# Kernel tuning notes

Hardware: AMD Instinct MI355X
Metric: run time of the kernel (lower is better)

## Reference

```python
import jax, jax.numpy as jnp
import numpy as np

S = 128          # shared sequence length of v/q/a/k
D = 512          # model dim
H = 8            # n_heads
W = D // H       # head width (becomes the v/q/a einsum axes)
NUM = S // 8     # num_v = num_q = num_a = num_k
SCALE = float(np.sqrt(H))  # source divides by sqrt(a.size(-1)) == sqrt(n_heads)


def _heads(x):
    # split_last(x,(H,-1)).transpose(1,2) on a 2D (S,D) tensor -> (S, W, H)
    return x.reshape(S, H, W).transpose(0, 2, 1)


def setup_inputs() -> dict:
    key = jax.random.key(0)
    ks = jax.random.split(key, 24)
    d = {}
    for i, n in enumerate(['v', 'q', 'a', 'k']):
        d[n] = jax.random.normal(ks[i], (S, D), jnp.float32)
    for n in ['v_mask', 'q_mask', 'a_mask', 'k_mask']:
        d[n] = jnp.ones((S,), jnp.bool_)
    wnames = ['Wv', 'Wq', 'Wa', 'Wk', 'Wvo', 'Wqo', 'Wao', 'Wko']
    bnames = ['bv', 'bq', 'ba', 'bk', 'bvo', 'bqo', 'bao', 'bko']
    for i, (wn, bn) in enumerate(zip(wnames, bnames)):
        d[wn] = jax.random.normal(ks[4 + 2 * i], (D, D), jnp.float32) / np.sqrt(D)
        d[bn] = jax.random.normal(ks[5 + 2 * i], (D,), jnp.float32) * 0.01
    return d


def reference(v, q, a, k, v_mask, q_mask, a_mask, k_mask,
              Wv, bv, Wq, bq, Wa, ba, Wk, bk,
              Wvo, bvo, Wqo, bqo, Wao, bao, Wko, bko):
    # input projections (torch Linear: x @ W.T + b)
    vp = v @ Wv.T + bv
    qp = q @ Wq.T + bq
    ap = a @ Wa.T + ba
    kp = k @ Wk.T + bk
    # output projections are applied to the already-projected tensors
    vo = vp @ Wvo.T + bvo
    qo = qp @ Wqo.T + bqo
    ao = ap @ Wao.T + bao
    ko = kp @ Wko.T + bko
    tv, tq, ta, tk = map(_heads, (vp, qp, ap, kp))      # (S, W, H)
    tvo, tqo, tao, tko = map(_heads, (vo, qo, ao, ko))  # (S, W, H)
    # trilinear scores: in source labels b=1, h=S, v/q/a in W, w=H
    att = jnp.einsum('sic,sjc,slc->sijl', tv, tq, ta) / SCALE   # (S, W, W, W)
    att1 = jnp.einsum('sic,sjc,slc->sijl', tv, tq, tk) / SCALE  # (S, W, W, W)
    # joint softmax over the flat num_v*num_q*num_a axis (flat memory reshape,
    # exactly like torch .view); dropout p=0.0 -> identity
    scores = jax.nn.softmax(att.reshape(-1, H, NUM * NUM * NUM), axis=-1)
    scores = scores.reshape(-1, H, NUM, NUM, NUM)  # stored as self.scores in torch
    # output contractions use the UNNORMALIZED att1 (as in the source)
    v_res = jnp.einsum('sijl,sic->isc', att1, tvo).reshape(1, W, S * H)
    q_res = jnp.einsum('sijl,sjc->jsc', att1, tqo).reshape(1, W, S * H)
    a_res = jnp.einsum('sijl,slc->lsc', att1, tao).reshape(1, W, S * H)
    k_res = tko[None].reshape(1, S, W * H)
    return (v_res, q_res, a_res, k_res, scores)
```

## Files before the change

kernel.cpp:

```cpp
#include <hip/hip_runtime.h>
#include <hip/hip_bf16.h>

#define INV_SCALE 0.35355339059327373f

struct Proj4Args {
  const float* x[4];
  const float* w[4];
  const float* b[4];
  float* y[4];
};

__device__ __forceinline__ void gemm8_body(const float* xg, const float* wg_p,
                                           const float* bp, int dbase, int t,
                                           float* SH, float o[4]) {
  const int s = t & 127;
  const int h = t >> 7;
  float* WL = SH;
  float(*XT)[129] = (float(*)[129])(SH + 4096);
  {
    const float4* wg = (const float4*)(wg_p + dbase * 512);
    float4* wl4 = (float4*)WL;
#pragma unroll
    for (int r = 0; r < 4; ++r) wl4[t + r * 256] = wg[t + r * 256];
  }
  const int row = t >> 3;
  const int col = t & 7;
  float acc[4] = {0.f, 0.f, 0.f, 0.f};
  float4 pre[4];
#pragma unroll
  for (int r = 0; r < 4; ++r)
    pre[r] = ((const float4*)(xg + (row + r * 32) * 512))[col];
  for (int c = 0; c < 16; ++c) {
    __syncthreads();
#pragma unroll
    for (int r = 0; r < 4; ++r) {
      float4 f = pre[r];
      int rr = row + r * 32;
      XT[col * 4 + 0][rr] = f.x;
      XT[col * 4 + 1][rr] = f.y;
      XT[col * 4 + 2][rr] = f.z;
      XT[col * 4 + 3][rr] = f.w;
    }
    __syncthreads();
    if (c + 1 < 16) {
#pragma unroll
      for (int r = 0; r < 4; ++r)
        pre[r] = ((const float4*)(xg + (row + r * 32) * 512))[(c + 1) * 8 + col];
    }
#pragma unroll
    for (int k4 = 0; k4 < 8; ++k4) {
      float xv0 = XT[k4 * 4 + 0][s];
      float xv1 = XT[k4 * 4 + 1][s];
      float xv2 = XT[k4 * 4 + 2][s];
      float xv3 = XT[k4 * 4 + 3][s];
#pragma unroll
      for (int di = 0; di < 4; ++di) {
        const float4 wv =
            *(const float4*)&WL[(h * 4 + di) * 512 + c * 32 + k4 * 4];
        acc[di] = fmaf(wv.x, xv0, acc[di]);
        acc[di] = fmaf(wv.y, xv1, acc[di]);
        acc[di] = fmaf(wv.z, xv2, acc[di]);
        acc[di] = fmaf(wv.w, xv3, acc[di]);
      }
    }
  }
#pragma unroll
  for (int di = 0; di < 4; ++di) o[di] = acc[di] + bp[dbase + h * 4 + di];
}

__global__ __launch_bounds__(256) void proj4_kernel(Proj4Args A) {
  __shared__ float SH[8224];
  const int blk = blockIdx.x;
  const int p = blk >> 6;
  const int dbase = (blk & 63) * 8;
  const int t = threadIdx.x;
  float o[4];
  gemm8_body(A.x[p], A.w[p], A.b[p], dbase, t, SH, o);
  const int s = t & 127;
  const int h = t >> 7;
  *(float4*)(A.y[p] + s * 512 + dbase + h * 4) = make_float4(o[0], o[1], o[2], o[3]);
}

struct FusedArgs {
  const float* w2[4];
  const float* b2[4];
  const float* vp;
  const float* qp;
  const float* ap;
  const float* kp;
  float* out;
};

__device__ __forceinline__ void proj2_direct_body(const FusedArgs& F, int blk,
                                                  int t, float* SH) {
  const int p = blk >> 6;
  const int dbase = (blk & 63) * 8;
  const float* xsrc[4] = {F.vp, F.qp, F.ap, F.kp};
  float o[4];
  gemm8_body(xsrc[p], F.w2[p], F.b2[p], dbase, t, SH, o);
  const int s = t & 127;
  const int h = t >> 7;
  const int c_head = dbase >> 6;
  const int i0 = (dbase & 63) + h * 4;
  if (p == 3) {
#pragma unroll
    for (int di = 0; di < 4; ++di)
      F.out[196608 + s * 512 + (i0 + di) * 8 + c_head] = o[di];
    return;
  }
  const float* fac = (p == 0) ? F.vp : (p == 1) ? F.qp : F.kp;
  const float* S0 = (p == 0) ? F.qp : F.vp;
  const float* S1 = (p == 2) ? F.qp : F.kp;
  __syncthreads();
  float* Sm = SH;
#pragma unroll
  for (int m = 0; m < 2; ++m) {
    const float* M = m ? S1 : S0;
#pragma unroll
    for (int cc = 0; cc < 4; ++cc) {
      const int c = h * 4 + cc;
      const float4* r4 = (const float4*)(M + s * 512 + c * 64);
      float sum = 0.f;
#pragma unroll
      for (int u = 0; u < 16; ++u) {
        float4 f = r4[u];
        sum += (f.x + f.y) + (f.z + f.w);
      }
      Sm[m * 1024 + s * 8 + c] = sum;
    }
  }
  __syncthreads();
  float prod[8];
#pragma unroll
  for (int c = 0; c < 8; ++c)
    prod[c] = Sm[s * 8 + c] * Sm[1024 + s * 8 + c];
#pragma unroll
  for (int di = 0; di < 4; ++di) {
    const int i = i0 + di;
    float A1 = 0.f;
#pragma unroll
    for (int c = 0; c < 8; ++c)
      A1 = fmaf(fac[s * 512 + c * 64 + i], prod[c], A1);
    F.out[p * 65536 + i * 1024 + s * 8 + c_head] = o[di] * (A1 * INV_SCALE);
  }
}

__device__ __forceinline__ void scores_body(const float* __restrict__ vp,
                                            const float* __restrict__ qp,
                                            const float* __restrict__ ap,
                                            float* __restrict__ out, int b,
                                            int t, float* SH) {
  const int s = b >> 4;
  const int i0 = (b & 15) * 4;
  float* tqL = SH;
  float* taL = SH + 512;
  float* uL = SH + 1024;
  float(*redM)[4] = (float(*)[4])(SH + 1056);
  float(*redS)[4] = (float(*)[4])(SH + 1072);
  {
    const float* qr = qp + s * 512;
    const float* ar = ap + s * 512;
    tqL[t] = qr[t]; tqL[t + 256] = qr[t + 256];
    taL[t] = ar[t]; taL[t + 256] = ar[t + 256];
    if (t < 32) {
      int ii = t >> 3, c = t & 7;
      uL[t] = vp[s * 512 + c * 64 + i0 + ii] * INV_SCALE;
    }
  }
  __syncthreads();
  const int j0 = t >> 3;
  const int l0 = (t & 7) * 8;
  float acc[4][16];
#pragma unroll
  for (int ii = 0; ii < 4; ++ii)
#pragma unroll
    for (int x = 0; x < 16; ++x) acc[ii][x] = 0.f;
#pragma unroll
  for (int c = 0; c < 8; ++c) {
    float t0 = tqL[c * 64 + j0];
    float t1 = tqL[c * 64 + j0 + 32];
    float4 A0 = *reinterpret_cast<const float4*>(&taL[c * 64 + l0]);
    float4 A1v = *reinterpret_cast<const float4*>(&taL[c * 64 + l0 + 4]);
    float ta8[8] = {A0.x, A0.y, A0.z, A0.w, A1v.x, A1v.y, A1v.z, A1v.w};
#pragma unroll
    for (int ii = 0; ii < 4; ++ii) {
      float uv = uL[ii * 8 + c];
      float m0 = uv * t0;
      float m1 = uv * t1;
#pragma unroll
      for (int x = 0; x < 8; ++x) {
        acc[ii][x] = fmaf(m0, ta8[x], acc[ii][x]);
        acc[ii][8 + x] = fmaf(m1, ta8[x], acc[ii][8 + x]);
      }
    }
  }
  const int wid = t >> 6, ln = t & 63;
#pragma unroll
  for (int ii = 0; ii < 4; ++ii) {
    float m = acc[ii][0];
#pragma unroll
    for (int x = 1; x < 16; ++x) m = fmaxf(m, acc[ii][x]);
#pragma unroll
    for (int o = 32; o; o >>= 1) m = fmaxf(m, __shfl_xor(m, o));
    if (ln == 0) redM[ii][wid] = m;
  }
  __syncthreads();
#pragma unroll
  for (int ii = 0; ii < 4; ++ii) {
    float mf = fmaxf(fmaxf(redM[ii][0], redM[ii][1]),
                     fmaxf(redM[ii][2], redM[ii][3]));
    float sl = 0.f;
#pragma unroll
    for (int x = 0; x < 16; ++x) {
      float e = __expf(acc[ii][x] - mf);
      acc[ii][x] = e;
      sl += e;
    }
#pragma unroll
    for (int o = 32; o; o >>= 1) sl += __shfl_xor(sl, o);
    if (ln == 0) redS[ii][wid] = sl;
  }
  __syncthreads();
  const long sbase = 262144L + (long)s * 262144 + (long)i0 * 4096;
#pragma unroll
  for (int ii = 0; ii < 4; ++ii) {
    float tot = (redS[ii][0] + redS[ii][1]) + (redS[ii][2] + redS[ii][3]);
    float sc = 1.0f / tot;
#pragma unroll
    for (int jj = 0; jj < 2; ++jj) {
      float4* pp = reinterpret_cast<float4*>(
          out + sbase + ii * 4096 + (j0 + jj * 32) * 64 + l0);
      pp[0] = make_float4(acc[ii][jj * 8 + 0] * sc, acc[ii][jj * 8 + 1] * sc,
                          acc[ii][jj * 8 + 2] * sc, acc[ii][jj * 8 + 3] * sc);
      pp[1] = make_float4(acc[ii][jj * 8 + 4] * sc, acc[ii][jj * 8 + 5] * sc,
                          acc[ii][jj * 8 + 6] * sc, acc[ii][jj * 8 + 7] * sc);
    }
  }
}

__global__ __launch_bounds__(256) void fused_kernel(FusedArgs F) {
  __shared__ float SH[8224];
  const int b = blockIdx.x;
  if (b < 256)
    proj2_direct_body(F, b, threadIdx.x, SH);
  else
    scores_body(F.vp, F.qp, F.ap, F.out, b - 256, threadIdx.x, SH);
}

extern "C" void kernel_launch(void* const* d_in, const int* in_sizes, int n_in,
                              void* d_out, int out_size, void* d_ws, size_t ws_size,
                              hipStream_t stream) {
  int wb = 8;
  if (n_in >= 5 && in_sizes[4] == 262144) wb = 4;
  const float* W[8];
  const float* B[8];
  for (int i = 0; i < 8; ++i) {
    W[i] = (const float*)d_in[wb + 2 * i];
    B[i] = (const float*)d_in[wb + 2 * i + 1];
  }
  float* ws = (float*)d_ws;
  float* vp = ws;
  float* qp = ws + 65536;
  float* ap = ws + 131072;
  float* kp = ws + 196608;
  float* out = (float*)d_out;

  Proj4Args a1;
  for (int i = 0; i < 4; ++i) {
    a1.x[i] = (const float*)d_in[i];
    a1.w[i] = W[i];
    a1.b[i] = B[i];
  }
  a1.y[0] = vp; a1.y[1] = qp; a1.y[2] = ap; a1.y[3] = kp;
  hipLaunchKernelGGL(proj4_kernel, dim3(256), dim3(256), 0, stream, a1);

  FusedArgs F;
  for (int i = 0; i < 4; ++i) {
    F.w2[i] = W[4 + i];
    F.b2[i] = B[4 + i];
  }
  F.vp = vp; F.qp = qp; F.ap = ap; F.kp = kp; F.out = out;
  hipLaunchKernelGGL(fused_kernel, dim3(2304), dim3(256), 0, stream, F);
}
```

Before: 233.8 us.

## Drop softmax max pass, use exp2 with prescaled factor, row-major X tile

```diff
diff --git a/kernel.cpp b/kernel.cpp
--- a/kernel.cpp
+++ b/kernel.cpp
@@ -1,7 +1,8 @@
 #include <hip/hip_runtime.h>
-#include <hip/hip_bf16.h>
+#include <math.h>
 
 #define INV_SCALE 0.35355339059327373f
+#define LOG2E 1.4426950408889634f
 
 struct Proj4Args {
   const float* x[4];
@@ -10,13 +11,15 @@
   float* y[4];
 };
 
-__device__ __forceinline__ void gemm8_body(const float* xg, const float* wg_p,
-                                           const float* bp, int dbase, int t,
-                                           float* SH, float o[4]) {
+__device__ __forceinline__ void gemm8_body(const float* __restrict__ xg,
+                                           const float* __restrict__ wg_p,
+                                           const float* __restrict__ bp,
+                                           int dbase, int t, float* SH,
+                                           float o[4]) {
   const int s = t & 127;
   const int h = t >> 7;
   float* WL = SH;
-  float(*XT)[129] = (float(*)[129])(SH + 4096);
+  float(*XL)[36] = (float(*)[36])(SH + 4096);
   {
     const float4* wg = (const float4*)(wg_p + dbase * 512);
     float4* wl4 = (float4*)WL;
@@ -33,14 +36,8 @@
   for (int c = 0; c < 16; ++c) {
     __syncthreads();
 #pragma unroll
-    for (int r = 0; r < 4; ++r) {
-      float4 f = pre[r];
-      int rr = row + r * 32;
-      XT[col * 4 + 0][rr] = f.x;
-      XT[col * 4 + 1][rr] = f.y;
-      XT[col * 4 + 2][rr] = f.z;
-      XT[col * 4 + 3][rr] = f.w;
-    }
+    for (int r = 0; r < 4; ++r)
+      *(float4*)&XL[row + r * 32][col * 4] = pre[r];
     __syncthreads();
     if (c + 1 < 16) {
 #pragma unroll
@@ -49,18 +46,15 @@
     }
 #pragma unroll
     for (int k4 = 0; k4 < 8; ++k4) {
-      float xv0 = XT[k4 * 4 + 0][s];
-      float xv1 = XT[k4 * 4 + 1][s];
-      float xv2 = XT[k4 * 4 + 2][s];
-      float xv3 = XT[k4 * 4 + 3][s];
+      const float4 xv = *(const float4*)&XL[s][k4 * 4];
 #pragma unroll
       for (int di = 0; di < 4; ++di) {
         const float4 wv =
             *(const float4*)&WL[(h * 4 + di) * 512 + c * 32 + k4 * 4];
-        acc[di] = fmaf(wv.x, xv0, acc[di]);
-        acc[di] = fmaf(wv.y, xv1, acc[di]);
-        acc[di] = fmaf(wv.z, xv2, acc[di]);
-        acc[di] = fmaf(wv.w, xv3, acc[di]);
+        acc[di] = fmaf(wv.x, xv.x, acc[di]);
+        acc[di] = fmaf(wv.y, xv.y, acc[di]);
+        acc[di] = fmaf(wv.z, xv.z, acc[di]);
+        acc[di] = fmaf(wv.w, xv.w, acc[di]);
       }
     }
   }
@@ -69,7 +63,7 @@
 }
 
 __global__ __launch_bounds__(256) void proj4_kernel(Proj4Args A) {
-  __shared__ float SH[8224];
+  __shared__ float SH[8704];
   const int blk = blockIdx.x;
   const int p = blk >> 6;
   const int dbase = (blk & 63) * 8;
@@ -155,17 +149,14 @@
   float* tqL = SH;
   float* taL = SH + 512;
   float* uL = SH + 1024;
-  float(*redM)[4] = (float(*)[4])(SH + 1056);
-  float(*redS)[4] = (float(*)[4])(SH + 1072);
-  {
-    const float* qr = qp + s * 512;
-    const float* ar = ap + s * 512;
-    tqL[t] = qr[t]; tqL[t + 256] = qr[t + 256];
-    taL[t] = ar[t]; taL[t + 256] = ar[t + 256];
-    if (t < 32) {
-      int ii = t >> 3, c = t & 7;
-      uL[t] = vp[s * 512 + c * 64 + i0 + ii] * INV_SCALE;
-    }
+  float(*redS)[4] = (float(*)[4])(SH + 1056);
+  if (t < 128)
+    ((float4*)tqL)[t] = ((const float4*)(qp + s * 512))[t];
+  else
+    ((float4*)taL)[t - 128] = ((const float4*)(ap + s * 512))[t - 128];
+  if (t < 32) {
+    int ii = t >> 3, c = t & 7;
+    uL[t] = vp[s * 512 + c * 64 + i0 + ii] * (INV_SCALE * LOG2E);
   }
   __syncthreads();
   const int j0 = t >> 3;
@@ -197,22 +188,10 @@
   const int wid = t >> 6, ln = t & 63;
 #pragma unroll
   for (int ii = 0; ii < 4; ++ii) {
-    float m = acc[ii][0];
-#pragma unroll
-    for (int x = 1; x < 16; ++x) m = fmaxf(m, acc[ii][x]);
-#pragma unroll
-    for (int o = 32; o; o >>= 1) m = fmaxf(m, __shfl_xor(m, o));
-    if (ln == 0) redM[ii][wid] = m;
-  }
-  __syncthreads();
-#pragma unroll
-  for (int ii = 0; ii < 4; ++ii) {
-    float mf = fmaxf(fmaxf(redM[ii][0], redM[ii][1]),
-                     fmaxf(redM[ii][2], redM[ii][3]));
     float sl = 0.f;
 #pragma unroll
     for (int x = 0; x < 16; ++x) {
-      float e = __expf(acc[ii][x] - mf);
+      float e = exp2f(acc[ii][x]);
       acc[ii][x] = e;
       sl += e;
     }
@@ -239,7 +218,7 @@
 }
 
 __global__ __launch_bounds__(256) void fused_kernel(FusedArgs F) {
-  __shared__ float SH[8224];
+  __shared__ float SH[8704];
   const int b = blockIdx.x;
   if (b < 256)
     proj2_direct_body(F, b, threadIdx.x, SH);
```

Result: slower. 292.7 us (+25.2%).
